# Kernel tuning notes

Hardware: AMD Instinct MI355X
Metric: run time of the kernel (lower is better)

The kernel has to match this reference:

```python
import jax, jax.numpy as jnp
import numpy as np

HIDDEN = 2048
FFN = 8192
NUM_EXPERTS = 8
TOP_K = 2


def setup_inputs() -> dict:
    key = jax.random.key(0)
    ks = jax.random.split(key, 6)
    scale_h = 1.0 / np.sqrt(HIDDEN)
    scale_f = 1.0 / np.sqrt(FFN)
    return {
        "hidden_states": jax.random.normal(ks[0], (4, 2048, HIDDEN), jnp.float32),
        "gate_w": jax.random.normal(ks[1], (NUM_EXPERTS, HIDDEN), jnp.float32) * scale_h,
        "w1": jax.random.normal(ks[2], (NUM_EXPERTS, HIDDEN, FFN), jnp.float32) * scale_h,
        "b1": jax.random.normal(ks[3], (NUM_EXPERTS, FFN), jnp.float32) * 0.01,
        "w2": jax.random.normal(ks[4], (NUM_EXPERTS, FFN, HIDDEN), jnp.float32) * scale_f,
        "b2": jax.random.normal(ks[5], (NUM_EXPERTS, HIDDEN), jnp.float32) * 0.01,
    }


def reference(hidden_states, gate_w, w1, b1, w2, b2):
    B, S, H = hidden_states.shape
    E = gate_w.shape[0]
    tokens = hidden_states.reshape(-1, H)  # [T, H]

    # Router: softmax gate, top-2, renormalize selected weights
    logits = tokens @ gate_w.T  # [T, E]
    probs = jax.nn.softmax(logits, axis=-1)
    topk_w, topk_idx = jax.lax.top_k(probs, TOP_K)  # [T, 2]
    topk_w = topk_w / jnp.sum(topk_w, axis=-1, keepdims=True)

    # Dense combine weights: w_dense[t, e] = routing weight of token t for expert e
    w_dense = jnp.sum(jax.nn.one_hot(topk_idx, E, dtype=topk_w.dtype) * topk_w[..., None], axis=1)  # [T, E]

    # Per-expert FFN (exact GELU as nn.GELU default), weighted scatter-combine
    combined = jnp.zeros_like(tokens)
    for e in range(E):  # small fixed expert count
        h = jax.nn.gelu(tokens @ w1[e] + b1[e], approximate=False)  # [T, F]
        combined = combined + w_dense[:, e:e + 1] * (h @ w2[e] + b2[e])

    return combined.reshape(B, S, H) + hidden_states
```

## Files before the change

### kernel.cpp

```cpp
#include <hip/hip_runtime.h>
#include <hip/hip_bf16.h>

#define T_TOK 8192
#define HID 2048
#define FFN_ 8192
#define NE 8
#define MAXR 18432

typedef __attribute__((ext_vector_type(8))) short bf16x8;
typedef __attribute__((ext_vector_type(4))) float f32x4;
typedef __attribute__((ext_vector_type(8))) unsigned short u16x8;

__device__ __forceinline__ unsigned short f2bf(float f) {
  unsigned int u = __float_as_uint(f);
  u += 0x7fffu + ((u >> 16) & 1u);
  return (unsigned short)(u >> 16);
}
__device__ __forceinline__ float bf2f(unsigned short h) {
  return __uint_as_float(((unsigned int)h) << 16);
}

__device__ __forceinline__ void gload_lds16(const ushort* g, ushort* l) {
  __builtin_amdgcn_global_load_lds(
      (const __attribute__((address_space(1))) unsigned int*)g,
      (__attribute__((address_space(3))) unsigned int*)l, 16, 0, 0);
}

__device__ __forceinline__ float gelu_f(float v) {
  float u = v * (0.7978845608f + 0.0356774081f * v * v);
  float a = fabsf(u);
  float ex = __expf(-2.f * a);
  float r = 1.f / (1.f + ex);
  float th = (1.f - ex) * r;
  th = (u >= 0.f) ? th : -th;
  return 0.5f * v * (1.f + th);
}

__global__ __launch_bounds__(256) void router_kernel(
    const float* __restrict__ x, const float* __restrict__ gw,
    int* __restrict__ topk_idx, float* __restrict__ topk_w, int* __restrict__ counts)
{
  int lane = threadIdx.x & 63;
  int w = threadIdx.x >> 6;
  int t = blockIdx.x * 4 + w;
  const float* xr = x + (size_t)t * HID;
  float acc[NE];
#pragma unroll
  for (int e = 0; e < NE; ++e) acc[e] = 0.f;
  for (int h = lane; h < HID; h += 64) {
    float xv = xr[h];
#pragma unroll
    for (int e = 0; e < NE; ++e) acc[e] = fmaf(xv, gw[e * HID + h], acc[e]);
  }
#pragma unroll
  for (int e = 0; e < NE; ++e) {
#pragma unroll
    for (int s = 32; s > 0; s >>= 1) acc[e] += __shfl_xor(acc[e], s);
  }
  if (lane == 0) {
    int i0 = 0; float v0 = acc[0];
#pragma unroll
    for (int e = 1; e < NE; ++e) { if (acc[e] > v0) { v0 = acc[e]; i0 = e; } }
    int i1 = -1; float v1 = -3.4e38f;
#pragma unroll
    for (int e = 0; e < NE; ++e) { if (e != i0 && acc[e] > v1) { v1 = acc[e]; i1 = e; } }
    float r = __expf(v1 - v0);
    float w0 = 1.f / (1.f + r);
    float w1 = r * w0;
    topk_idx[2 * t] = i0; topk_idx[2 * t + 1] = i1;
    topk_w[2 * t] = w0;   topk_w[2 * t + 1] = w1;
    atomicAdd(&counts[i0], 1);
    atomicAdd(&counts[i1], 1);
  }
}

__global__ void offsets_kernel(const int* __restrict__ counts, int* __restrict__ offs) {
  if (threadIdx.x == 0 && blockIdx.x == 0) {
    int o = 0;
#pragma unroll
    for (int e = 0; e < NE; ++e) { offs[e] = o; o += (counts[e] + 255) & ~255; }
    offs[NE] = o;
  }
}

__global__ __launch_bounds__(256) void scatter_kernel(
    const int* __restrict__ topk_idx, const float* __restrict__ topk_w,
    const int* __restrict__ offs, int* __restrict__ cursors,
    int* __restrict__ slot_token, float* __restrict__ slot_w, int* __restrict__ token_slot)
{
  int t = blockIdx.x * blockDim.x + threadIdx.x;
  if (t >= T_TOK) return;
#pragma unroll
  for (int k = 0; k < 2; ++k) {
    int e = topk_idx[2 * t + k];
    int pos = atomicAdd(&cursors[e], 1);
    int slot = offs[e] + pos;
    slot_token[slot] = t;
    slot_w[slot] = topk_w[2 * t + k];
    token_slot[2 * t + k] = slot;
  }
}

__global__ __launch_bounds__(256) void gather_kernel(
    const float* __restrict__ x, const int* __restrict__ slot_token, ushort* __restrict__ Xg)
{
  int row = blockIdx.x;
  int tok = slot_token[row];
  ushort* dst = Xg + (size_t)row * HID + threadIdx.x * 8;
  if (tok < 0) {
    u16x8 z = {0, 0, 0, 0, 0, 0, 0, 0};
    *(u16x8*)dst = z;
  } else {
    const float* s = x + (size_t)tok * HID + threadIdx.x * 8;
    float4 a = *(const float4*)s;
    float4 b = *(const float4*)(s + 4);
    u16x8 v;
    v[0] = f2bf(a.x); v[1] = f2bf(a.y); v[2] = f2bf(a.z); v[3] = f2bf(a.w);
    v[4] = f2bf(b.x); v[5] = f2bf(b.y); v[6] = f2bf(b.z); v[7] = f2bf(b.w);
    *(u16x8*)dst = v;
  }
}

__global__ __launch_bounds__(512) void wconvert_kernel(
    const float* __restrict__ src0, ushort* __restrict__ dst0, int R, int C)
{
  __shared__ ushort tile[64][524];
  const int spr = C >> 9;
  const int spe = (R >> 6) * spr;
  int b = blockIdx.x;
  const int e = b / spe;
  const int s = b - e * spe;
  const int r0 = (s / spr) << 6;
  const int c0 = (s - (s / spr) * spr) << 9;
  const float* src = src0 + (size_t)e * R * C;
  ushort* dst = dst0 + (size_t)e * R * C;
  const int t = threadIdx.x;

#pragma unroll
  for (int i = 0; i < 16; ++i) {
    int idx = (i << 9) + t;
    int row = idx >> 7;
    int c4 = (idx & 127) << 2;
    float4 v = *(const float4*)&src[(size_t)(r0 + row) * C + c0 + c4];
    ushort4 u;
    u.x = f2bf(v.x); u.y = f2bf(v.y); u.z = f2bf(v.z); u.w = f2bf(v.w);
    *(ushort4*)&tile[row][c4] = u;
  }
  __syncthreads();
#pragma unroll
  for (int i = 0; i < 8; ++i) {
    int idx = (i << 9) + t;
    int c = idx >> 3;
    int r8 = (idx & 7) << 3;
    u16x8 o;
#pragma unroll
    for (int j = 0; j < 8; ++j) o[j] = tile[r8 + j][c];
    *(u16x8*)&dst[(size_t)(c0 + c) * R + r0 + r8] = o;
  }
}


#define VMWG() do { if constexpr (TM == 256) asm volatile("s_waitcnt vmcnt(6)" ::: "memory"); \
                    else                     asm volatile("s_waitcnt vmcnt(5)" ::: "memory"); } while (0)
#define VMW0() do { asm volatile("s_waitcnt vmcnt(0)" ::: "memory"); } while (0)
#define SCB()  __builtin_amdgcn_sched_barrier(0)
#define BAR()  __builtin_amdgcn_s_barrier()

#define STG_A(BUF, HALF, T) do {                                            \
    ushort* _d = lds + (BUF) * BUFS + (HALF) * REGA + tid * 8;              \
    gload_lds16(sA0 + (size_t)(HALF) * HOFFA + (size_t)(T) * 64, _d);       \
    if constexpr (TM == 256)                                                \
      gload_lds16(sA1 + (size_t)(HALF) * HOFFA + (size_t)(T) * 64, _d + 4096); \
  } while (0)
#define STG_B(BUF, HALF, T) do {                                            \
    ushort* _d = lds + (BUF) * BUFS + 2 * REGA + (HALF) * 8192 + tid * 8;   \
    gload_lds16(sB0 + (size_t)(HALF) * 32 * K + (size_t)(T) * 64, _d);      \
    gload_lds16(sB1 + (size_t)(HALF) * 32 * K + (size_t)(T) * 64, _d + 4096); \
  } while (0)

#define LDA(BUF, MQ) do {                                                   \
    _Pragma("unroll") for (int mm = 0; mm < MA; ++mm) {                     \
      const ushort* _p = lds + (BUF) * BUFS + (MQ) * REGA + aoff + mm * 1024; \
      af[mm][0] = *(const bf16x8*)(_p + ck0);                               \
      af[mm][1] = *(const bf16x8*)(_p + ck1);                               \
    } } while (0)
#define LDB(BUF, NQ) do {                                                   \
    _Pragma("unroll") for (int nn = 0; nn < 2; ++nn) {                      \
      const ushort* _p = lds + (BUF) * BUFS + 2 * REGA + (NQ) * 8192 + boff + nn * 1024; \
      bf[NQ][nn][0] = *(const bf16x8*)(_p + ck0);                           \
      bf[NQ][nn][1] = *(const bf16x8*)(_p + ck1);                           \
    } } while (0)

#define MM(MQ, NQ) do {                                                     \
    __builtin_amdgcn_s_setprio(1);                                          \
    _Pragma("unroll") for (int mm = 0; mm < MA; ++mm)                       \
    _Pragma("unroll") for (int nn = 0; nn < 2; ++nn) {                      \
      acc[(MQ)*MA+mm][(NQ)*2+nn] = __builtin_amdgcn_mfma_f32_16x16x32_bf16( \
          af[mm][0], bf[NQ][nn][0], acc[(MQ)*MA+mm][(NQ)*2+nn], 0, 0, 0);   \
      acc[(MQ)*MA+mm][(NQ)*2+nn] = __builtin_amdgcn_mfma_f32_16x16x32_bf16( \
          af[mm][1], bf[NQ][nn][1], acc[(MQ)*MA+mm][(NQ)*2+nn], 0, 0, 0);   \
    }                                                                       \
    __builtin_amdgcn_s_setprio(0);                                          \
  } while (0)

template <int EPI, int TM>
__global__ __launch_bounds__(512, 2) void gemm256_kernel(
    const ushort* __restrict__ A, const ushort* __restrict__ Bt,
    const float* __restrict__ bias, ushort* __restrict__ Cout,
    const float* __restrict__ slot_w, const int* __restrict__ offs,
    int K, int N, int gy)
{
  constexpr int REGA = TM * 32;
  constexpr int BUFS = 2 * REGA + 16384;
  constexpr int MA = TM / 64;
  constexpr int HOFFA_ROWS = TM / 4;
  __shared__ ushort lds[2 * BUFS];

  const int tid = threadIdx.x;
  const size_t HOFFA = (size_t)HOFFA_ROWS * K;
  int nwg = gridDim.x;
  int wg = blockIdx.x;
  int cpx = nwg >> 3;
  wg = (wg & 7) * cpx + (wg >> 3);
  int cb = wg / gy;
  int rb = wg - cb * gy;

  int total = offs[NE];
  int row0 = rb * TM;
  if (row0 >= total) return;
  int e = 0;
#pragma unroll
  for (int i = 1; i < NE; ++i) e += (row0 >= offs[i]) ? 1 : 0;

  const ushort* Ag = A + (size_t)row0 * K;
  const ushort* Bg = Bt + ((size_t)e * N + (size_t)cb * 256) * K;

  const int pr0 = tid >> 3;
  const int pr1 = 64 + pr0;
  const int j0 = (tid & 7) ^ (pr0 & 7);
  const int j1 = (tid & 7) ^ (pr1 & 7);
  const int rA0 = (TM == 256) ? pr0 : (((pr0 >> 5) << 6) + (pr0 & 31));
  const int rA1 = 128 + pr0;
  const int rB0 = ((pr0 >> 5) << 6) + (pr0 & 31);
  const int rB1 = ((pr1 >> 5) << 6) + (pr1 & 31);
  const ushort* sA0 = Ag + (size_t)rA0 * K + j0 * 8;
  const ushort* sA1 = Ag + (size_t)rA1 * K + j1 * 8;
  const ushort* sB0 = Bg + (size_t)rB0 * K + j0 * 8;
  const ushort* sB1 = Bg + (size_t)rB1 * K + j1 * 8;

  const int lane = tid & 63;
  const int wid = tid >> 6;
  const int wr = wid >> 2, wc = wid & 3;
  const int lrow = lane & 15, g = lane >> 4, x7 = lrow & 7;
  const int ck0 = (g ^ x7) * 8;
  const int ck1 = ((4 + g) ^ x7) * 8;
  const int aoff = (wr * (TM / 4) + lrow) * 64;
  const int boff = (wc * 32 + lrow) * 64;

  f32x4 acc[TM / 32][4] = {};
  bf16x8 af[MA][2], bf[2][2][2];

  const int NT = K >> 6;
  const int NITER = NT >> 1;

  STG_A(0, 0, 0); STG_A(0, 1, 0); STG_B(0, 0, 0); STG_B(0, 1, 0);
  STG_A(1, 0, 1); STG_B(1, 0, 1); STG_B(1, 1, 1);
  VMWG();
  BAR(); SCB();

  for (int it = 0; it < NITER; ++it) {
    const int tb = 2 * it + 1;
    const int tn0 = 2 * it + 2;
    const int tn1 = 2 * it + 3;
    const bool more0 = tn0 < NT;
    const bool more1 = tn1 < NT;
    const bool last = (it + 1 == NITER);

    STG_A(1, 1, tb);
    LDA(0, 0); LDB(0, 0);
    LDB(0, 1);
    MM(0, 0);
    MM(0, 1);
    BAR(); SCB();

    if (more0) { STG_A(0, 0, tn0); STG_B(0, 0, tn0); }
    LDA(0, 1);
    MM(1, 0);
    if (more0) STG_B(0, 1, tn0);
    MM(1, 1);
    if (last) { VMW0(); } else { VMWG(); }
    BAR(); SCB();

    if (more0) STG_A(0, 1, tn0);
    LDA(1, 0); LDB(1, 0);
    LDB(1, 1);
    MM(0, 0);
    MM(0, 1);
    BAR(); SCB();

    if (more1) { STG_A(1, 0, tn1); STG_B(1, 0, tn1); }
    LDA(1, 1);
    MM(1, 0);
    if (more1) STG_B(1, 1, tn1);
    MM(1, 1);
    if (more1) VMWG();
    BAR(); SCB();
  }

  const int colb = cb * 256 + wc * 64;
  const int rowb = row0 + wr * (TM / 2);
  float bv[4];
#pragma unroll
  for (int n = 0; n < 4; ++n)
    bv[n] = bias[(size_t)e * N + colb + n * 16 + lrow];
#pragma unroll
  for (int m = 0; m < TM / 32; ++m) {
    const int mq = m / MA, mm = m % MA;
    const int gr = rowb + mq * (TM / 4) + mm * 16 + g * 4;
#pragma unroll
    for (int i = 0; i < 4; ++i) {
      const int grow = gr + i;
      float sw = (EPI == 1) ? slot_w[grow] : 0.f;
      ushort* crow = Cout + (size_t)grow * N + colb + lrow;
#pragma unroll
      for (int n = 0; n < 4; ++n) {
        float v = acc[m][n][i] + bv[n];
        if (EPI == 0) v = gelu_f(v);
        else          v *= sw;
        crow[n * 16] = f2bf(v);
      }
    }
  }
}

__global__ __launch_bounds__(256) void combine_kernel(
    const float* __restrict__ x, const ushort* __restrict__ Yp,
    const int* __restrict__ token_slot, float* __restrict__ out)
{
  int t = blockIdx.x;
  int s0 = token_slot[2 * t], s1 = token_slot[2 * t + 1];
  int c = threadIdx.x * 8;
  const float* xr = x + (size_t)t * HID + c;
  u16x8 y0 = *(const u16x8*)&Yp[(size_t)s0 * HID + c];
  u16x8 y1 = *(const u16x8*)&Yp[(size_t)s1 * HID + c];
  float4 xa = *(const float4*)xr;
  float4 xb = *(const float4*)(xr + 4);
  float4 oa, ob;
  oa.x = xa.x + bf2f(y0[0]) + bf2f(y1[0]);
  oa.y = xa.y + bf2f(y0[1]) + bf2f(y1[1]);
  oa.z = xa.z + bf2f(y0[2]) + bf2f(y1[2]);
  oa.w = xa.w + bf2f(y0[3]) + bf2f(y1[3]);
  ob.x = xb.x + bf2f(y0[4]) + bf2f(y1[4]);
  ob.y = xb.y + bf2f(y0[5]) + bf2f(y1[5]);
  ob.z = xb.z + bf2f(y0[6]) + bf2f(y1[6]);
  ob.w = xb.w + bf2f(y0[7]) + bf2f(y1[7]);
  float* orow = out + (size_t)t * HID + c;
  *(float4*)orow = oa;
  *(float4*)(orow + 4) = ob;
}

extern "C" void kernel_launch(void* const* d_in, const int* in_sizes, int n_in,
                              void* d_out, int out_size, void* d_ws, size_t ws_size,
                              hipStream_t stream)
{
  const float* x  = (const float*)d_in[0];
  const float* gw = (const float*)d_in[1];
  const float* w1 = (const float*)d_in[2];
  const float* b1 = (const float*)d_in[3];
  const float* w2 = (const float*)d_in[4];
  const float* b2 = (const float*)d_in[5];
  float* out = (float*)d_out;

  char* ws = (char*)d_ws;
  ushort* wT  = (ushort*)(ws + 0);
  ushort* Hb  = (ushort*)(ws + 268435456);
  ushort* Xg  = (ushort*)(ws + 570425344);
  ushort* Yp  = Xg;
  char* sm = ws + 645922816;
  int*   slot_token = (int*)(sm);
  float* slot_w     = (float*)(sm + 73728);
  int*   token_slot = (int*)(sm + 147456);
  int*   topk_idx   = (int*)(sm + 212992);
  float* topk_w     = (float*)(sm + 278528);
  int*   counts     = (int*)(sm + 344064);
  int*   cursors    = (int*)(sm + 344096);
  int*   offs       = (int*)(sm + 344128);

  hipMemsetAsync(counts, 0, 64, stream);
  hipMemsetAsync(slot_token, 0xFF, MAXR * 4, stream);

  router_kernel<<<dim3(T_TOK / 4), dim3(256), 0, stream>>>(x, gw, topk_idx, topk_w, counts);
  offsets_kernel<<<dim3(1), dim3(64), 0, stream>>>(counts, offs);
  scatter_kernel<<<dim3(T_TOK / 256), dim3(256), 0, stream>>>(
      topk_idx, topk_w, offs, cursors, slot_token, slot_w, token_slot);
  gather_kernel<<<dim3(MAXR), dim3(256), 0, stream>>>(x, slot_token, Xg);

  wconvert_kernel<<<dim3(4096), dim3(512), 0, stream>>>(w1, wT, HID, FFN_);
  gemm256_kernel<0, 256><<<dim3((FFN_ / 256) * (MAXR / 256)), dim3(512), 0, stream>>>(
      Xg, wT, b1, Hb, nullptr, offs, HID, FFN_, MAXR / 256);

  wconvert_kernel<<<dim3(4096), dim3(512), 0, stream>>>(w2, wT, FFN_, HID);
  gemm256_kernel<1, 128><<<dim3((HID / 256) * (MAXR / 128)), dim3(512), 0, stream>>>(
      Hb, wT, b2, Yp, slot_w, offs, FFN_, HID, MAXR / 128);

  combine_kernel<<<dim3(T_TOK), dim3(256), 0, stream>>>(x, Yp, token_slot, out);
}
```

Baseline: 1.856 ms.

## Fuse w2 weight conversion into GEMM1 launch to overlap with tail blocks

Merges the first expert GEMM and the w2 fp32-to-bf16 transpose-convert into one grid. Blocks beyond the GEMM count run the conversion, which writes to a separate workspace region so it cannot clobber the w1 copy still being read. The aim is to fill the GEMM's tail and idle CUs with bandwidth-bound conversion work and to drop one kernel boundary. The fused kernel reserves the larger LDS size for every block, and the path only runs when the workspace is big enough, with the old sequence kept as a fallback.

```diff
diff --git a/kernel.cpp b/kernel.cpp
--- a/kernel.cpp
+++ b/kernel.cpp
@@ -121,13 +121,13 @@
   }
 }
 
-__global__ __launch_bounds__(512) void wconvert_kernel(
-    const float* __restrict__ src0, ushort* __restrict__ dst0, int R, int C)
-{
-  __shared__ ushort tile[64][524];
+__device__ __forceinline__ void wconv_body(
+    ushort* ldsbuf, const float* __restrict__ src0, ushort* __restrict__ dst0,
+    int R, int C, int b)
+{
+  ushort (*tile)[524] = (ushort (*)[524])ldsbuf;
   const int spr = C >> 9;
   const int spe = (R >> 6) * spr;
-  int b = blockIdx.x;
   const int e = b / spe;
   const int s = b - e * spe;
   const int r0 = (s / spr) << 6;
@@ -157,6 +157,13 @@
     for (int j = 0; j < 8; ++j) o[j] = tile[r8 + j][c];
     *(u16x8*)&dst[(size_t)(c0 + c) * R + r0 + r8] = o;
   }
+}
+
+__global__ __launch_bounds__(512) void wconvert_kernel(
+    const float* __restrict__ src0, ushort* __restrict__ dst0, int R, int C)
+{
+  __shared__ ushort lds[64 * 524];
+  wconv_body(lds, src0, dst0, R, C, blockIdx.x);
 }
 
 
@@ -204,22 +211,21 @@
   } while (0)
 
 template <int EPI, int TM>
-__global__ __launch_bounds__(512, 2) void gemm256_kernel(
+__device__ __forceinline__ void gemm_body(
+    ushort* lds,
     const ushort* __restrict__ A, const ushort* __restrict__ Bt,
     const float* __restrict__ bias, ushort* __restrict__ Cout,
     const float* __restrict__ slot_w, const int* __restrict__ offs,
-    int K, int N, int gy)
+    int K, int N, int gy, int nwg, int bidx)
 {
   constexpr int REGA = TM * 32;
   constexpr int BUFS = 2 * REGA + 16384;
   constexpr int MA = TM / 64;
   constexpr int HOFFA_ROWS = TM / 4;
-  __shared__ ushort lds[2 * BUFS];
 
   const int tid = threadIdx.x;
   const size_t HOFFA = (size_t)HOFFA_ROWS * K;
-  int nwg = gridDim.x;
-  int wg = blockIdx.x;
+  int wg = bidx;
   int cpx = nwg >> 3;
   wg = (wg & 7) * cpx + (wg >> 3);
   int cb = wg / gy;
@@ -331,6 +337,32 @@
       }
     }
   }
+}
+
+template <int EPI, int TM>
+__global__ __launch_bounds__(512, 2) void gemm256_kernel(
+    const ushort* __restrict__ A, const ushort* __restrict__ Bt,
+    const float* __restrict__ bias, ushort* __restrict__ Cout,
+    const float* __restrict__ slot_w, const int* __restrict__ offs,
+    int K, int N, int gy)
+{
+  __shared__ ushort lds[TM * 128 + 32768];
+  gemm_body<EPI, TM>(lds, A, Bt, bias, Cout, slot_w, offs, K, N, gy,
+                     (int)gridDim.x, (int)blockIdx.x);
+}
+
+__global__ __launch_bounds__(512, 2) void gemm1_conv_kernel(
+    const ushort* __restrict__ A, const ushort* __restrict__ Bt,
+    const float* __restrict__ bias, ushort* __restrict__ Cout,
+    const int* __restrict__ offs,
+    const float* __restrict__ w2, ushort* __restrict__ w2t, int gemmBlocks)
+{
+  __shared__ ushort lds[65536];
+  if ((int)blockIdx.x < gemmBlocks)
+    gemm_body<0, 256>(lds, A, Bt, bias, Cout, nullptr, offs, HID, FFN_,
+                      MAXR / 256, gemmBlocks, (int)blockIdx.x);
+  else
+    wconv_body(lds, w2, w2t, FFN_, HID, (int)blockIdx.x - gemmBlocks);
 }
 
 __global__ __launch_bounds__(256) void combine_kernel(
@@ -386,6 +418,10 @@
   int*   cursors    = (int*)(sm + 344096);
   int*   offs       = (int*)(sm + 344128);
 
+  const size_t W2T_OFF = 646267136ULL;
+  const bool fused = ws_size >= W2T_OFF + 268435456ULL;
+  ushort* w2t = fused ? (ushort*)(ws + W2T_OFF) : wT;
+
   hipMemsetAsync(counts, 0, 64, stream);
   hipMemsetAsync(slot_token, 0xFF, MAXR * 4, stream);
 
@@ -396,12 +432,18 @@
   gather_kernel<<<dim3(MAXR), dim3(256), 0, stream>>>(x, slot_token, Xg);
 
   wconvert_kernel<<<dim3(4096), dim3(512), 0, stream>>>(w1, wT, HID, FFN_);
-  gemm256_kernel<0, 256><<<dim3((FFN_ / 256) * (MAXR / 256)), dim3(512), 0, stream>>>(
-      Xg, wT, b1, Hb, nullptr, offs, HID, FFN_, MAXR / 256);
-
-  wconvert_kernel<<<dim3(4096), dim3(512), 0, stream>>>(w2, wT, FFN_, HID);
-  gemm256_kernel<1, 128><<<dim3((HID / 256) * (MAXR / 128)), dim3(512), 0, stream>>>(
-      Hb, wT, b2, Yp, slot_w, offs, FFN_, HID, MAXR / 128);
+
+  if (fused) {
+    gemm1_conv_kernel<<<dim3(2304 + 4096), dim3(512), 0, stream>>>(
+        Xg, wT, b1, Hb, offs, w2, w2t, 2304);
+  } else {
+    gemm256_kernel<0, 256><<<dim3(2304), dim3(512), 0, stream>>>(
+        Xg, wT, b1, Hb, nullptr, offs, HID, FFN_, MAXR / 256);
+    wconvert_kernel<<<dim3(4096), dim3(512), 0, stream>>>(w2, wT, FFN_, HID);
+  }
+
+  gemm256_kernel<1, 128><<<dim3(1152), dim3(512), 0, stream>>>(
+      Hb, w2t, b2, Yp, slot_w, offs, FFN_, HID, MAXR / 128);
 
   combine_kernel<<<dim3(T_TOK), dim3(256), 0, stream>>>(x, Yp, token_slot, out);
 }
```

Measured after the change: 1.815 ms. -2.2%, faster.
